# Kernel optimization log

Measured on AMD Instinct MI355X. Metric: run time of the kernel, lower is better.

The kernel has to match this reference:

```python
import jax, jax.numpy as jnp
import numpy as np

B, N, E = 4, 10000, 100000
C_IN = 16              # 16x0e input scalars
N_EDGE_FEAT = 128
MUL0, MUL1 = 16, 8     # out_irreps = 16x0e + 8x1o -> dim 16 + 24 = 40
W_NUMEL = C_IN * MUL0 + C_IN * MUL1  # 384
MODES = 2
OUT_DIM = MUL0 + 3 * MUL1
ALPHA = 1.0 / np.sqrt(float(C_IN))   # e3nn element path normalization (fan_in = mul_in*mul_sh = 16)
BN_EPS = 1e-5


def setup_inputs() -> dict:
    key = jax.random.key(0)
    ks = jax.random.split(key, 12)
    x = jax.random.normal(ks[0], (B, N, C_IN), jnp.float32)
    edge_index = jax.random.randint(ks[1], (2, E), 0, N)
    edge_attr = jax.random.normal(ks[2], (B, E, N_EDGE_FEAT), jnp.float32)
    edge_sh = jax.random.normal(ks[3], (B, E, 4), jnp.float32)
    scale = 1.0 / (C_IN * MUL0)
    tc_wr = scale * jax.random.uniform(ks[4], (C_IN, MUL0, MODES), jnp.float32)
    tc_wi = scale * jax.random.uniform(ks[5], (C_IN, MUL0, MODES), jnp.float32)
    mlp_w1 = jax.random.normal(ks[6], (N_EDGE_FEAT, N_EDGE_FEAT), jnp.float32) / np.sqrt(N_EDGE_FEAT)
    mlp_b1 = jnp.zeros((N_EDGE_FEAT,), jnp.float32)
    mlp_w2 = jax.random.normal(ks[7], (N_EDGE_FEAT, W_NUMEL), jnp.float32) / np.sqrt(N_EDGE_FEAT)
    mlp_b2 = jnp.zeros((W_NUMEL,), jnp.float32)
    bn_gamma = jnp.ones((OUT_DIM,), jnp.float32)
    bn_beta = jnp.zeros((OUT_DIM,), jnp.float32)
    return dict(x=x, edge_index=edge_index, edge_attr=edge_attr, edge_sh=edge_sh,
                tc_wr=tc_wr, tc_wi=tc_wi, mlp_w1=mlp_w1, mlp_b1=mlp_b1,
                mlp_w2=mlp_w2, mlp_b2=mlp_b2, bn_gamma=bn_gamma, bn_beta=bn_beta)


def reference(x, edge_index, edge_attr, edge_sh, tc_wr, tc_wi,
              mlp_w1, mlp_b1, mlp_w2, mlp_b2, bn_gamma, bn_beta):
    Bx, Nx, _ = x.shape
    # --- SimplifiedSpectralConv1d over the batch (time) axis ---
    n_fft = min(8, Bx)
    W = tc_wr + 1j * tc_wi                       # [C_IN, MUL0, MODES] complex64
    x_ft = jnp.fft.rfft(x, n=n_fft, axis=0)      # [n_fft//2+1, N, C_IN]
    out_ft = jnp.zeros((x_ft.shape[0], Nx, MUL0), dtype=x_ft.dtype)
    out_ft = out_ft.at[:MODES].set(jnp.einsum('bni,iom->bno', x_ft[:MODES], W))
    xs = jnp.fft.irfft(out_ft, n=n_fft, axis=0)
    if xs.shape[0] < Bx:
        xs = jnp.pad(xs, ((0, Bx - xs.shape[0]), (0, 0), (0, 0)))
    x = xs[:Bx]                                   # [B, N, MUL0] (scalar block fully replaced)

    # --- per-edge weights from edge MLP ---
    h = jax.nn.relu(edge_attr @ mlp_w1 + mlp_b1)
    ew = h @ mlp_w2 + mlp_b2                      # [B, E, 384]
    w1 = ew[..., :C_IN * MUL0].reshape(Bx, E, C_IN, MUL0)
    w2 = ew[..., C_IN * MUL0:].reshape(Bx, E, C_IN, MUL1)

    # --- gather + fully connected tensor product (0e x 0e -> 0e, 0e x 1o -> 1o) ---
    src, dst = edge_index[0], edge_index[1]
    xg = x[:, src]                                # [B, E, C_IN]
    sh0 = edge_sh[..., 0]                         # [B, E]
    sh1 = edge_sh[..., 1:4]                       # [B, E, 3]
    out0 = jnp.einsum('bei,beio->beo', xg * sh0[..., None], w1) * ALPHA          # [B,E,16]
    out1 = (jnp.einsum('bei,beio,bem->beom', xg, w2, sh1) * ALPHA).reshape(Bx, E, 3 * MUL1)
    msg = jnp.concatenate([out0, out1], axis=-1)  # [B, E, 40]

    # --- scatter-mean into destination nodes ---
    seg_sum = jax.vmap(lambda m: jax.ops.segment_sum(m, dst, num_segments=Nx))(msg)
    cnt = jax.ops.segment_sum(jnp.ones((E,), msg.dtype), dst, num_segments=Nx)
    agg = seg_sum / jnp.maximum(cnt, 1.0)[None, :, None]   # [B, N, 40]

    # --- BatchNorm1d (training-mode batch statistics) over flattened B*N ---
    flat = agg.reshape(-1, OUT_DIM)
    mu = flat.mean(axis=0)
    var = flat.var(axis=0)
    out = (agg - mu) * jax.lax.rsqrt(var + BN_EPS) * bn_gamma + bn_beta
    return out
```

## Files before the change

### kernel.cpp

```cpp
#include <hip/hip_runtime.h>

#define B_CNT 4
#define N_CNT 10000
#define E_CNT 100000

typedef __attribute__((ext_vector_type(8))) short s16x8;
typedef __attribute__((ext_vector_type(4))) float f32x4;
typedef __attribute__((ext_vector_type(4))) unsigned int u32x4;

__device__ __forceinline__ float b2f(unsigned short u) {
  union { unsigned int i; float f; } v; v.i = ((unsigned int)u) << 16; return v.f;
}
__device__ __forceinline__ unsigned short f2b(float f) {
  union { float f; unsigned int i; } v; v.f = f;
  unsigned int b = v.i;
  b += 0x7FFFu + ((b >> 16) & 1u);
  return (unsigned short)(b >> 16);
}
__device__ __forceinline__ unsigned int cvtpk(float lo, float hi) {
  unsigned int r;
  asm("v_cvt_pk_bf16_f32 %0, %1, %2" : "=v"(r) : "v"(lo), "v"(hi));
  return r;
}
__device__ __forceinline__ void keeps(s16x8 v) {
  u32x4 u = __builtin_bit_cast(u32x4, v);
  asm volatile("" :: "v"(u.x), "v"(u.y), "v"(u.z), "v"(u.w));
}
__device__ __forceinline__ void gld16(const void* g, void* l) {
  __builtin_amdgcn_global_load_lds(
      (const __attribute__((address_space(1))) unsigned int*)g,
      (__attribute__((address_space(3))) unsigned int*)l, 16, 0, 0);
}

__global__ void k_prep(const float* __restrict__ x,
                       const float* __restrict__ tcwr,
                       const float* __restrict__ tcwi,
                       float* __restrict__ xnew,
                       const float* __restrict__ w1,
                       const float* __restrict__ w2,
                       unsigned short* __restrict__ pw1,
                       unsigned short* __restrict__ pw2,
                       const int* __restrict__ eidx,
                       int* __restrict__ cnt) {
  const int bid = blockIdx.x;
  const int t = threadIdx.x;
  if (bid < 40) {
    __shared__ float Wr[256], Wi[256];
    Wr[t] = tcwr[t * 2] + tcwr[t * 2 + 1];
    Wi[t] = tcwi[t * 2] + tcwi[t * 2 + 1];
    __syncthreads();
    const int n = bid * 256 + t;
    if (n >= N_CNT) return;
    float xt[4][16];
    for (int tt = 0; tt < 4; ++tt) {
      const float* xp = x + ((size_t)tt * N_CNT + n) * 16;
#pragma unroll
      for (int i0 = 0; i0 < 16; i0 += 4) {
        const float4 v = *(const float4*)(xp + i0);
        xt[tt][i0 + 0] = v.x; xt[tt][i0 + 1] = v.y;
        xt[tt][i0 + 2] = v.z; xt[tt][i0 + 3] = v.w;
      }
    }
    float s[16], a[16], bb[16];
#pragma unroll
    for (int i = 0; i < 16; ++i) {
      s[i]  = xt[0][i] + xt[1][i] + xt[2][i] + xt[3][i];
      a[i]  = xt[0][i] - xt[2][i];
      bb[i] = xt[1][i] - xt[3][i];
    }
    for (int o = 0; o < 16; ++o) {
      float r0 = 0.f, p = 0.f, qq = 0.f;
#pragma unroll
      for (int i = 0; i < 16; ++i) {
        const float wr = Wr[i * 16 + o], wi = Wi[i * 16 + o];
        r0 += s[i] * wr;
        p  += a[i] * wr + bb[i] * wi;
        qq += a[i] * wi - bb[i] * wr;
      }
      xnew[((size_t)0 * N_CNT + n) * 16 + o] = 0.25f * (r0 + 2.f * p);
      xnew[((size_t)1 * N_CNT + n) * 16 + o] = 0.25f * (r0 - 2.f * qq);
      xnew[((size_t)2 * N_CNT + n) * 16 + o] = 0.25f * (r0 - 2.f * p);
      xnew[((size_t)3 * N_CNT + n) * 16 + o] = 0.25f * (r0 + 2.f * qq);
    }
  } else if (bid < 72) {
    const int tg = (bid - 40) * 256 + t;
    const int tile = tg >> 6, l = tg & 63, q = l >> 4, lm = l & 15;
    if (tile < 32) {
      const int nt = tile >> 2, kk = tile & 3;
      const int n = nt * 16 + lm;
      unsigned short* dst = pw1 + ((size_t)tile * 64 + l) * 8;
#pragma unroll
      for (int j = 0; j < 8; ++j) dst[j] = f2b(w1[(kk * 32 + q * 8 + j) * 128 + n]);
    } else {
      const int t2 = tile - 32;
      const int nt = t2 >> 2, kk = t2 & 3;
      int col;
      if (nt < 16) col = nt * 16 + lm;
      else col = 256 + (8 * (lm & 1) + (nt - 16)) * 8 + (lm >> 1);
      unsigned short* dst = pw2 + ((size_t)t2 * 64 + l) * 8;
#pragma unroll
      for (int j = 0; j < 8; ++j) dst[j] = f2b(w2[(kk * 32 + q * 8 + j) * 384 + col]);
    }
  } else {
    const int e = (bid - 72) * 256 + t;
    if (e < E_CNT) atomicAdd(&cnt[eidx[E_CNT + e]], 1);
  }
}

__global__ void k_scan(const int* __restrict__ cnt, int* __restrict__ rowstart,
                       int* __restrict__ runoff) {
  __shared__ int partial[256];
  const int t = threadIdx.x;
  const int c0 = t * 40;
  int s = 0;
  for (int j = 0; j < 40; ++j) {
    const int idx = c0 + j;
    if (idx < N_CNT) s += cnt[idx];
  }
  partial[t] = s;
  __syncthreads();
  if (t == 0) {
    int acc = 0;
    for (int i = 0; i < 256; ++i) { const int v = partial[i]; partial[i] = acc; acc += v; }
  }
  __syncthreads();
  int acc = partial[t];
  for (int j = 0; j < 40; ++j) {
    const int idx = c0 + j;
    if (idx < N_CNT) { rowstart[idx] = acc; runoff[idx] = acc; acc += cnt[idx]; }
  }
  if (t == 255) rowstart[N_CNT] = acc;
}

__global__ void k_pos(const int* __restrict__ eidx, int* __restrict__ runoff,
                      int* __restrict__ pos) {
  const int e = blockIdx.x * 256 + threadIdx.x;
  if (e < E_CNT) pos[e] = atomicAdd(&runoff[eidx[E_CNT + e]], 1);
}

template <bool ATOMIC>
__global__ __launch_bounds__(256, 4) void k_edge(
    const float* __restrict__ ea, const int* __restrict__ eidx,
    const float* __restrict__ esh,
    const unsigned short* __restrict__ pw1, const unsigned short* __restrict__ pw2,
    const float* __restrict__ b1v, const float* __restrict__ b2v,
    const float* __restrict__ xnew, const int* __restrict__ idx_arr,
    float* __restrict__ out_base, const size_t bstride) {
  __shared__ __align__(16) unsigned short U[32 * 392];
  __shared__ __align__(16) unsigned short Hs[32 * 136];
  __shared__ float xgs[32 * 20];
  __shared__ float shs[32 * 4];
  __shared__ int ids[32];
  unsigned short* const EWt = U;
  const float* const Af = (const float*)U;

  const int t = threadIdx.x;
  const int b = blockIdx.y;
  const int e0 = blockIdx.x * 32;
  const int w = t >> 6, l = t & 63, q = l >> 4, lm = l & 15;

  const float* eab = ea + (size_t)b * E_CNT * 128;
#pragma unroll
  for (int i = 0; i < 4; ++i) {
    const int p = i * 256 + w * 64 + l;
    const int e = p >> 5;
    const int g = (p & 31) ^ (e & 7);
    const float* src = eab + ((size_t)(e0 + e)) * 128 + g * 4;
    char* dst = (char*)U + (i * 4096 + w * 1024);
    gld16(src, dst);
  }

  if (t < 128) {
    const int el = t >> 2, i0 = (t & 3) * 4;
    const int src = eidx[e0 + el];
    const float4 v = *(const float4*)(xnew + ((size_t)b * N_CNT + src) * 16 + i0);
    xgs[el * 20 + i0 + 0] = v.x;
    xgs[el * 20 + i0 + 1] = v.y;
    xgs[el * 20 + i0 + 2] = v.z;
    xgs[el * 20 + i0 + 3] = v.w;
  } else if (t < 160) {
    const int el = t - 128;
    const float4 v = *(const float4*)(esh + ((size_t)b * E_CNT + e0 + el) * 4);
    shs[el * 4 + 0] = v.x;
    shs[el * 4 + 1] = v.y;
    shs[el * 4 + 2] = v.z;
    shs[el * 4 + 3] = v.w;
  } else if (t < 192) {
    const int el = t - 160;
    ids[el] = idx_arr[e0 + el];
  }

  s16x8 bfr[2][4];
#pragma unroll
  for (int j = 0; j < 2; ++j)
#pragma unroll
    for (int kk = 0; kk < 4; ++kk)
      bfr[j][kk] = *(const s16x8*)(pw1 + (((size_t)(2 * w + j) * 4 + kk) * 64 + l) * 8);

  __syncthreads();

  f32x4 acc1[2][2];
#pragma unroll
  for (int mt = 0; mt < 2; ++mt)
#pragma unroll
    for (int j = 0; j < 2; ++j) acc1[mt][j] = (f32x4)0.0f;

  const int s7 = lm & 7;
#pragma unroll
  for (int kk = 0; kk < 4; ++kk) {
#pragma unroll
    for (int mt = 0; mt < 2; ++mt) {
      const int el = mt * 16 + lm;
      const int g1 = kk * 8 + q * 2;
      const float4 a0 = *(const float4*)&Af[el * 128 + ((g1 ^ s7) << 2)];
      const float4 a1 = *(const float4*)&Af[el * 128 + (((g1 + 1) ^ s7) << 2)];
      union { unsigned int u[4]; s16x8 s; } au;
      au.u[0] = cvtpk(a0.x, a0.y); au.u[1] = cvtpk(a0.z, a0.w);
      au.u[2] = cvtpk(a1.x, a1.y); au.u[3] = cvtpk(a1.z, a1.w);
      const s16x8 af = au.s;
      acc1[mt][0] = __builtin_amdgcn_mfma_f32_16x16x32_bf16(af, bfr[0][kk], acc1[mt][0], 0, 0, 0);
      acc1[mt][1] = __builtin_amdgcn_mfma_f32_16x16x32_bf16(af, bfr[1][kk], acc1[mt][1], 0, 0, 0);
    }
  }

  s16x8 bw0[6];
#pragma unroll
  for (int jj = 0; jj < 6; ++jj)
    bw0[jj] = *(const s16x8*)(pw2 + (((size_t)(6 * w + jj) * 4 + 0) * 64 + l) * 8);

#pragma unroll
  for (int j = 0; j < 2; ++j) {
    const int n = (2 * w + j) * 16 + lm;
    const float bias = b1v[n];
#pragma unroll
    for (int mt = 0; mt < 2; ++mt) {
#pragma unroll
      for (int r = 0; r < 4; r += 2) {
        const float v0 = fmaxf(acc1[mt][j][r] + bias, 0.0f);
        const float v1 = fmaxf(acc1[mt][j][r + 1] + bias, 0.0f);
        const unsigned int pr = cvtpk(v0, v1);
        Hs[(mt * 16 + q * 4 + r) * 136 + n] = (unsigned short)pr;
        Hs[(mt * 16 + q * 4 + r + 1) * 136 + n] = (unsigned short)(pr >> 16);
      }
    }
  }
#pragma unroll
  for (int jj = 0; jj < 6; ++jj) keeps(bw0[jj]);
  __syncthreads();

  f32x4 acc2[2][6];
#pragma unroll
  for (int mt = 0; mt < 2; ++mt)
#pragma unroll
    for (int jj = 0; jj < 6; ++jj) acc2[mt][jj] = (f32x4)0.0f;

#pragma unroll
  for (int kk = 0; kk < 4; ++kk) {
    s16x8 bw[6];
    if (kk == 0) {
#pragma unroll
      for (int jj = 0; jj < 6; ++jj) bw[jj] = bw0[jj];
    } else {
#pragma unroll
      for (int jj = 0; jj < 6; ++jj)
        bw[jj] = *(const s16x8*)(pw2 + (((size_t)(6 * w + jj) * 4 + kk) * 64 + l) * 8);
    }
#pragma unroll
    for (int mt = 0; mt < 2; ++mt) {
      const s16x8 ah = *(const s16x8*)(&Hs[(mt * 16 + lm) * 136 + kk * 32 + q * 8]);
#pragma unroll
      for (int jj = 0; jj < 6; ++jj)
        acc2[mt][jj] = __builtin_amdgcn_mfma_f32_16x16x32_bf16(ah, bw[jj], acc2[mt][jj], 0, 0, 0);
    }
  }

  float bias6[6];
#pragma unroll
  for (int jj = 0; jj < 6; ++jj) {
    const int T = 6 * w + jj;
    const int bcol = (T < 16) ? (T * 16 + lm)
                              : (256 + (8 * (l & 1) + (T - 16)) * 8 + (lm >> 1));
    bias6[jj] = b2v[bcol];
  }
  const int sq4 = (q & 1) * 4;
  const int nsq4 = 4 - sq4;
  const int ch2off = (16 + (lm >> 1)) * 8 + (((l & 1) ^ (q & 1)) ? 4 : 0);
#pragma unroll
  for (int mt = 0; mt < 2; ++mt)
#pragma unroll
    for (int r = 0; r < 4; ++r) {
      const int edge = mt * 16 + q * 4 + r;
      const unsigned int p0 = cvtpk(acc2[mt][0][r] + bias6[0], acc2[mt][1][r] + bias6[1]);
      const unsigned int p1 = cvtpk(acc2[mt][2][r] + bias6[2], acc2[mt][3][r] + bias6[3]);
      const unsigned int p2 = cvtpk(acc2[mt][4][r] + bias6[4], acc2[mt][5][r] + bias6[5]);
      unsigned int* base = (unsigned int*)&EWt[edge * 392];
      if (w == 0) {
        unsigned int* d = base + lm * 8 + sq4;
        d[0] = p0; d[1] = p1; d[2] = p2;
      } else if (w == 1) {
        base[lm * 8 + sq4 + 3] = p0;
        unsigned int* d = base + lm * 8 + nsq4;
        d[0] = p1; d[1] = p2;
      } else if (w == 2) {
        unsigned int* d = base + lm * 8 + nsq4 + 2;
        d[0] = p0; d[1] = p1;
        base[ch2off] = p2;
      } else {
        unsigned int* d = base + ch2off + 1;
        d[0] = p0; d[1] = p1; d[2] = p2;
      }
    }
  __syncthreads();

  {
    const int m = t >> 3, sub = t & 7;
    const int sqr8 = ((m >> 2) & 1) << 3;
    float xr[16];
#pragma unroll
    for (int i0 = 0; i0 < 16; i0 += 4) {
      const float4 v = *(const float4*)&xgs[m * 20 + i0];
      xr[i0] = v.x; xr[i0 + 1] = v.y; xr[i0 + 2] = v.z; xr[i0 + 3] = v.w;
    }
    const float sh0v = 0.25f * shs[m * 4 + 0];
    const float s1a = 0.25f * shs[m * 4 + 1];
    const float s1b = 0.25f * shs[m * 4 + 2];
    const float s1c = 0.25f * shs[m * 4 + 3];
    float* outp = out_base + (size_t)b * bstride + (size_t)ids[m] * 40;
#pragma unroll
    for (int dd = 0; dd < 3; ++dd) {
      const int d = sub * 3 + dd;
      const unsigned short* ep = &EWt[m * 392 + d * 16];
      const s16x8 eA = *(const s16x8*)(ep + sqr8);
      const s16x8 eB = *(const s16x8*)(ep + 8 - sqr8);
      float dotv = 0.f;
#pragma unroll
      for (int i = 0; i < 8; ++i) {
        dotv += xr[i] * b2f((unsigned short)eA[i]);
        dotv += xr[8 + i] * b2f((unsigned short)eB[i]);
      }
      if (d < 16) {
        const float val = dotv * sh0v;
        if (ATOMIC) atomicAdd(outp + d, val); else outp[d] = val;
      } else {
        const int c0 = 16 + (d - 16) * 3;
        if (ATOMIC) {
          atomicAdd(outp + c0 + 0, dotv * s1a);
          atomicAdd(outp + c0 + 1, dotv * s1b);
          atomicAdd(outp + c0 + 2, dotv * s1c);
        } else {
          outp[c0 + 0] = dotv * s1a;
          outp[c0 + 1] = dotv * s1b;
          outp[c0 + 2] = dotv * s1c;
        }
      }
    }
  }
}

__global__ void k_agg(float* __restrict__ sums, const int* __restrict__ cnt,
                      float* __restrict__ psum, float* __restrict__ psq) {
  __shared__ float ls[40], lq[40];
  const int t = threadIdx.x;
  if (t < 40) { ls[t] = 0.f; lq[t] = 0.f; }
  __syncthreads();
  const unsigned base = blockIdx.x * 2048u + t;
  for (int k2 = 0; k2 < 8; ++k2) {
    const unsigned idx = base + k2 * 256u;
    if (idx < 1600000u) {
      const unsigned row = idx / 40u;
      const unsigned node = row % 10000u;
      const float c = (float)cnt[node];
      const float v = sums[idx] / fmaxf(c, 1.f);
      sums[idx] = v;
      const unsigned ch = idx - row * 40u;
      atomicAdd(&ls[ch], v);
      atomicAdd(&lq[ch], v * v);
    }
  }
  __syncthreads();
  if (t < 40) {
    atomicAdd(&psum[t], ls[t]);
    atomicAdd(&psq[t], lq[t]);
  }
}

__global__ __launch_bounds__(256) void k_gather(
    const float* __restrict__ msgbuf, const int* __restrict__ rowstart,
    float* __restrict__ sums, float* __restrict__ psum, float* __restrict__ psq) {
  const int t = threadIdx.x;
  const int wid = t >> 6, ch = t & 63;
  if (ch >= 40) return;
  float lsum = 0.f, lsq = 0.f;
  for (int k = 0; k < 8; ++k) {
    const int p = blockIdx.x * 32 + wid * 8 + k;
    const int bb = p / 10000;
    const int node = p - bb * 10000;
    const int r0 = rowstart[node], r1 = rowstart[node + 1];
    const float* base = msgbuf + (size_t)bb * (E_CNT * 40) + ch;
    float v0 = 0.f, v1 = 0.f, v2 = 0.f, v3 = 0.f;
    int r = r0;
    for (; r + 4 <= r1; r += 4) {
      v0 += base[(size_t)(r + 0) * 40];
      v1 += base[(size_t)(r + 1) * 40];
      v2 += base[(size_t)(r + 2) * 40];
      v3 += base[(size_t)(r + 3) * 40];
    }
    for (; r < r1; ++r) v0 += base[(size_t)r * 40];
    float v = (v0 + v1) + (v2 + v3);
    v /= fmaxf((float)(r1 - r0), 1.f);
    sums[(size_t)p * 40 + ch] = v;
    lsum += v; lsq += v * v;
  }
  atomicAdd(&psum[ch], lsum);
  atomicAdd(&psq[ch], lsq);
}

__global__ void k_out(const float* __restrict__ agg,
                      const float* __restrict__ psum, const float* __restrict__ psq,
                      const float* __restrict__ gma, const float* __restrict__ bta,
                      float* __restrict__ outp) {
  __shared__ float sc[40], sh[40];
  const int t = threadIdx.x;
  if (t < 40) {
    const float inv = 1.0f / 40000.0f;
    const float mu = psum[t] * inv;
    const float var = psq[t] * inv - mu * mu;
    const float s = rsqrtf(fmaxf(var, 0.0f) + 1e-5f) * gma[t];
    sc[t] = s;
    sh[t] = bta[t] - mu * s;
  }
  __syncthreads();
  const unsigned base = blockIdx.x * 1024u + t;
#pragma unroll
  for (int k2 = 0; k2 < 4; ++k2) {
    const unsigned idx = base + k2 * 256u;
    if (idx < 1600000u) {
      const unsigned row = idx / 40u;
      const unsigned ch = idx - row * 40u;
      outp[idx] = agg[idx] * sc[ch] + sh[ch];
    }
  }
}

extern "C" void kernel_launch(void* const* d_in, const int* in_sizes, int n_in,
                              void* d_out, int out_size, void* d_ws, size_t ws_size,
                              hipStream_t stream) {
  (void)in_sizes; (void)n_in; (void)out_size;
  const float* x    = (const float*)d_in[0];
  const int*   eidx = (const int*)d_in[1];
  const float* ea   = (const float*)d_in[2];
  const float* esh  = (const float*)d_in[3];
  const float* tcwr = (const float*)d_in[4];
  const float* tcwi = (const float*)d_in[5];
  const float* w1   = (const float*)d_in[6];
  const float* b1   = (const float*)d_in[7];
  const float* w2   = (const float*)d_in[8];
  const float* b2   = (const float*)d_in[9];
  const float* gma  = (const float*)d_in[10];
  const float* bta  = (const float*)d_in[11];

  char* ws = (char*)d_ws;
  float*          sums     = (float*)(ws + 0);
  int*            cnt      = (int*)(ws + 6400000);
  float*          psum     = (float*)(ws + 6440000);
  float*          psq      = (float*)(ws + 6440160);
  float*          xnew     = (float*)(ws + 6440448);
  unsigned short* pw1      = (unsigned short*)(ws + 9000448);
  unsigned short* pw2      = (unsigned short*)(ws + 9033216);
  int*            rowstart = (int*)(ws + 9131840);
  int*            runoff   = (int*)(ws + 9171856);
  int*            pos      = (int*)(ws + 9211856);
  float*          msgbuf   = (float*)(ws + 9611904);

  const bool use_csr = ws_size >= (size_t)73611904;

  if (use_csr) {
    hipMemsetAsync(ws + 6400000, 0, 40320, stream);
    k_prep<<<dim3(463), dim3(256), 0, stream>>>(x, tcwr, tcwi, xnew, w1, w2,
                                                pw1, pw2, eidx, cnt);
    k_scan<<<dim3(1), dim3(256), 0, stream>>>(cnt, rowstart, runoff);
    k_pos<<<dim3(391), dim3(256), 0, stream>>>(eidx, runoff, pos);
    k_edge<false><<<dim3(E_CNT / 32, B_CNT), dim3(256), 0, stream>>>(
        ea, eidx, esh, pw1, pw2, b1, b2, xnew, pos, msgbuf, (size_t)E_CNT * 40);
    k_gather<<<dim3(1250), dim3(256), 0, stream>>>(msgbuf, rowstart, sums, psum, psq);
    k_out<<<dim3(1563), dim3(256), 0, stream>>>(sums, psum, psq, gma, bta, (float*)d_out);
  } else {
    hipMemsetAsync(ws, 0, 6440320, stream);
    k_prep<<<dim3(463), dim3(256), 0, stream>>>(x, tcwr, tcwi, xnew, w1, w2,
                                                pw1, pw2, eidx, cnt);
    k_edge<true><<<dim3(E_CNT / 32, B_CNT), dim3(256), 0, stream>>>(
        ea, eidx, esh, pw1, pw2, b1, b2, xnew, eidx + E_CNT, sums, (size_t)N_CNT * 40);
    k_agg<<<dim3(782), dim3(256), 0, stream>>>(sums, cnt, psum, psq);
    k_out<<<dim3(1563), dim3(256), 0, stream>>>(sums, psum, psq, gma, bta, (float*)d_out);
  }
}
```

Measured before the change: 589.1 us.

## Flatten CSR gather to full-wave contiguous loads and use warp-shuffle scan

k_gather now has all 64 lanes stride linearly over each node's contiguous segment of 40*deg floats, where before only 40 lanes did strided per-channel loads. Each lane keeps partial sums in 5 register slots, since the channel id repeats every 5 wave-strides, and reduces them into per-wave shared memory with LDS atomics. Batch-norm partial sums are combined per block before the global atomics, which cuts global atomic traffic by a factor of four. k_scan replaces the serial 256-entry scan on one thread with a wavefront shuffle scan, adding more code but little extra work.

```diff
diff --git a/kernel.cpp b/kernel.cpp
--- a/kernel.cpp
+++ b/kernel.cpp
@@ -109,22 +109,29 @@
 
 __global__ void k_scan(const int* __restrict__ cnt, int* __restrict__ rowstart,
                        int* __restrict__ runoff) {
-  __shared__ int partial[256];
+  __shared__ int wsum[4];
   const int t = threadIdx.x;
+  const int wid = t >> 6, ln = t & 63;
   const int c0 = t * 40;
   int s = 0;
   for (int j = 0; j < 40; ++j) {
     const int idx = c0 + j;
     if (idx < N_CNT) s += cnt[idx];
   }
-  partial[t] = s;
+  int v = s;
+#pragma unroll
+  for (int off = 1; off < 64; off <<= 1) {
+    const int u = __shfl_up(v, off);
+    if (ln >= off) v += u;
+  }
+  if (ln == 63) wsum[wid] = v;
   __syncthreads();
   if (t == 0) {
-    int acc = 0;
-    for (int i = 0; i < 256; ++i) { const int v = partial[i]; partial[i] = acc; acc += v; }
-  }
-  __syncthreads();
-  int acc = partial[t];
+    int a = 0;
+    for (int i = 0; i < 4; ++i) { const int tv = wsum[i]; wsum[i] = a; a += tv; }
+  }
+  __syncthreads();
+  int acc = v - s + wsum[wid];
   for (int j = 0; j < 40; ++j) {
     const int idx = c0 + j;
     if (idx < N_CNT) { rowstart[idx] = acc; runoff[idx] = acc; acc += cnt[idx]; }
@@ -387,32 +394,67 @@
 __global__ __launch_bounds__(256) void k_gather(
     const float* __restrict__ msgbuf, const int* __restrict__ rowstart,
     float* __restrict__ sums, float* __restrict__ psum, float* __restrict__ psq) {
+  __shared__ float lacc[4][40];
+  __shared__ float bsum[40], bsq[40];
   const int t = threadIdx.x;
-  const int wid = t >> 6, ch = t & 63;
-  if (ch >= 40) return;
-  float lsum = 0.f, lsq = 0.f;
+  const int wid = t >> 6, l = t & 63;
+  if (t < 40) { bsum[t] = 0.f; bsq[t] = 0.f; }
+  __syncthreads();
+
+  int chj[5];
+#pragma unroll
+  for (int j = 0; j < 5; ++j) {
+    int c = l + 24 * j;
+    if (c >= 120) c -= 120;
+    else if (c >= 80) c -= 80;
+    else if (c >= 40) c -= 40;
+    chj[j] = c;
+  }
+
+  float lpsum = 0.f, lpsq = 0.f;
   for (int k = 0; k < 8; ++k) {
     const int p = blockIdx.x * 32 + wid * 8 + k;
     const int bb = p / 10000;
     const int node = p - bb * 10000;
     const int r0 = rowstart[node], r1 = rowstart[node + 1];
-    const float* base = msgbuf + (size_t)bb * (E_CNT * 40) + ch;
-    float v0 = 0.f, v1 = 0.f, v2 = 0.f, v3 = 0.f;
-    int r = r0;
-    for (; r + 4 <= r1; r += 4) {
-      v0 += base[(size_t)(r + 0) * 40];
-      v1 += base[(size_t)(r + 1) * 40];
-      v2 += base[(size_t)(r + 2) * 40];
-      v3 += base[(size_t)(r + 3) * 40];
-    }
-    for (; r < r1; ++r) v0 += base[(size_t)r * 40];
-    float v = (v0 + v1) + (v2 + v3);
-    v /= fmaxf((float)(r1 - r0), 1.f);
-    sums[(size_t)p * 40 + ch] = v;
-    lsum += v; lsq += v * v;
-  }
-  atomicAdd(&psum[ch], lsum);
-  atomicAdd(&psq[ch], lsq);
+    const int d = r1 - r0;
+    const int L = d * 40;
+    const float* seg = msgbuf + (size_t)bb * (E_CNT * 40) + (size_t)r0 * 40;
+
+    if (l < 40) lacc[wid][l] = 0.f;
+
+    float racc[5] = {0.f, 0.f, 0.f, 0.f, 0.f};
+#pragma unroll
+    for (int i = 0; i < 16; ++i) {
+      const int base = l + i * 64;
+      if (base < L) racc[i % 5] += seg[base];
+    }
+    int base = l + 16 * 64;
+    while (base < L) {
+      racc[1] += seg[base]; base += 64;
+      if (base < L) { racc[2] += seg[base]; base += 64; } else break;
+      if (base < L) { racc[3] += seg[base]; base += 64; } else break;
+      if (base < L) { racc[4] += seg[base]; base += 64; } else break;
+      if (base < L) { racc[0] += seg[base]; base += 64; } else break;
+    }
+#pragma unroll
+    for (int j = 0; j < 5; ++j) atomicAdd(&lacc[wid][chj[j]], racc[j]);
+
+    if (l < 40) {
+      const float v = lacc[wid][l] / fmaxf((float)d, 1.0f);
+      sums[(size_t)p * 40 + l] = v;
+      lpsum += v; lpsq += v * v;
+    }
+  }
+  if (l < 40) {
+    atomicAdd(&bsum[l], lpsum);
+    atomicAdd(&bsq[l], lpsq);
+  }
+  __syncthreads();
+  if (t < 40) {
+    atomicAdd(&psum[t], bsum[t]);
+    atomicAdd(&psq[t], bsq[t]);
+  }
 }
 
 __global__ void k_out(const float* __restrict__ agg,
```

After: 511.7 us. -13.1%, faster.
